# Kernel optimization log

Hardware: AMD Instinct MI355X
Metric: run time of the kernel (lower is better)

Reference implementation:

```python
import jax, jax.numpy as jnp
import numpy as np

B, S, D, H, L, V = 4, 512, 1024, 16, 4, 32000
DH = D // H
LATENT_START, N_LATENT, LATENT_ID = 64, 6, 5


def _ln(x, g, b):
    m = x.mean(-1, keepdims=True)
    v = ((x - m) ** 2).mean(-1, keepdims=True)
    return (x - m) * jax.lax.rsqrt(v + 1e-5) * g + b


def _model(x_emb, pos_ids, pos_emb, Wqkv, Wo, W1, W2, ln1_g, ln1_b, ln2_g, ln2_b, lnf_g, lnf_b, lm_head):
    # x_emb: [B,T,D]; returns (last_hidden [B,T,D] after final LN, logits [B,T,V])
    b, T, _ = x_emb.shape
    x = x_emb + pos_emb[pos_ids]
    causal = jnp.tril(jnp.ones((T, T), bool))
    for l in range(L):
        h = _ln(x, ln1_g[l], ln1_b[l])
        q, k, v = jnp.split(h @ Wqkv[l], 3, axis=-1)
        q = q.reshape(b, T, H, DH).transpose(0, 2, 1, 3)
        k = k.reshape(b, T, H, DH).transpose(0, 2, 1, 3)
        v = v.reshape(b, T, H, DH).transpose(0, 2, 1, 3)
        scores = jnp.einsum('bhqd,bhkd->bhqk', q, k) / np.float32(np.sqrt(DH))
        scores = jnp.where(causal, scores, jnp.float32(-1e9))
        attn = jax.nn.softmax(scores, axis=-1)
        o = jnp.einsum('bhqk,bhkd->bhqd', attn, v).transpose(0, 2, 1, 3).reshape(b, T, D)
        x = x + o @ Wo[l]
        h2 = _ln(x, ln2_g[l], ln2_b[l])
        x = x + jax.nn.gelu(h2 @ W1[l]) @ W2[l]
    hid = _ln(x, lnf_g, lnf_b)  # GPT2 hidden_states[-1] is post ln_f
    return hid, hid @ lm_head


def setup_inputs() -> dict:
    key = jax.random.key(0)
    ks = jax.random.split(key, 10)
    input_ids = jax.random.randint(ks[0], (B, S), 0, V, dtype=jnp.int32)
    input_ids = input_ids.at[:, LATENT_START:LATENT_START + N_LATENT].set(LATENT_ID)
    attention_mask = jnp.ones((B, S), jnp.int32)
    labels = jax.random.randint(ks[1], (B, S), 0, V, dtype=jnp.int32)
    position_ids = jnp.broadcast_to(jnp.arange(S, dtype=jnp.int32), (B, S))
    s = 0.02
    return {
        'input_ids': input_ids, 'attention_mask': attention_mask,
        'labels': labels, 'position_ids': position_ids,
        'emb': jax.random.normal(ks[2], (V, D), jnp.float32) * s,
        'pos_emb': jax.random.normal(ks[3], (S, D), jnp.float32) * s,
        'Wqkv': jax.random.normal(ks[4], (L, D, 3 * D), jnp.float32) * s,
        'Wo': jax.random.normal(ks[5], (L, D, D), jnp.float32) * s,
        'W1': jax.random.normal(ks[6], (L, D, 4 * D), jnp.float32) * s,
        'W2': jax.random.normal(ks[7], (L, 4 * D, D), jnp.float32) * s,
        'ln1_g': jnp.ones((L, D), jnp.float32), 'ln1_b': jnp.zeros((L, D), jnp.float32),
        'ln2_g': jnp.ones((L, D), jnp.float32), 'ln2_b': jnp.zeros((L, D), jnp.float32),
        'lnf_g': jnp.ones((D,), jnp.float32), 'lnf_b': jnp.zeros((D,), jnp.float32),
        'lm_head': jax.random.normal(ks[8], (D, V), jnp.float32) * s,
    }


def reference(input_ids, attention_mask, labels, position_ids, emb, pos_emb, Wqkv, Wo, W1, W2, ln1_g, ln1_b, ln2_g, ln2_b, lnf_g, lnf_b, lm_head):
    params = (pos_emb, Wqkv, Wo, W1, W2, ln1_g, ln1_b, ln2_g, ln2_b, lnf_g, lnf_b, lm_head)
    inputs_embeds = emb[input_ids]  # [B,S,D]
    start, end = 0, LATENT_START
    logits_list = []
    for p in range(N_LATENT):  # iterative latent passes
        hid, lg = _model(inputs_embeds[:, :end], position_ids[:, :end], *params)
        logits_list.append(lg[:, start:end])
        pos = LATENT_START + p
        # vectorized scatter: splice previous-position hidden state into latent slot
        inputs_embeds = inputs_embeds.at[:, pos, :].set(hid[:, pos - 1, :])
        start, end = end, (S if p + 1 >= N_LATENT else end + 1)
    hid, lg = _model(inputs_embeds[:, :end], position_ids[:, :end], *params)
    logits_list.append(lg[:, start:end])
    logits = jnp.concatenate(logits_list, axis=1)  # [B,S,V]
    shift_logits = logits[:, :-1]
    shift_labels = labels[:, 1:]
    logp = jax.nn.log_softmax(shift_logits, axis=-1)
    loss = -jnp.take_along_axis(logp, shift_labels[..., None], axis=-1).mean()
    return loss, inputs_embeds, logits
```

## Files before the change

kernel.cpp:

```cpp
#include <hip/hip_runtime.h>

static constexpr int BB  = 4;
static constexpr int SS  = 512;
static constexpr int DD  = 1024;
static constexpr int HH  = 16;
static constexpr int LL  = 4;
static constexpr int VV  = 32000;
static constexpr int DHH = 64;
static constexpr int FFF = 4096;

typedef short bf16x8  __attribute__((ext_vector_type(8)));
typedef short bf16x4v __attribute__((ext_vector_type(4)));
typedef float f32x4   __attribute__((ext_vector_type(4)));

__device__ __forceinline__ float b2f(ushort u){
  union { float f; unsigned int u32; } x; x.u32 = ((unsigned int)u) << 16; return x.f;
}
__device__ __forceinline__ ushort f2b(float f){
  union { float f; unsigned int u32; } x; x.f = f;
  unsigned int u = x.u32;
  return (ushort)((u + 0x7FFFu + ((u >> 16) & 1u)) >> 16);
}

__global__ __launch_bounds__(256) void convT_k(const float* __restrict__ in, ushort* __restrict__ out,
                                               int K, int N, long inStride, long outStride)
{
  in  += (long)blockIdx.z * inStride;
  out += (long)blockIdx.z * outStride;
  __shared__ float tile[64][65];
  int n0 = blockIdx.x * 64, k0 = blockIdx.y * 64;
  int tid = threadIdx.x;
  int cc = tid & 63, rr = tid >> 6;
#pragma unroll
  for (int i = 0; i < 16; i++){
    int r = rr + i * 4;
    tile[r][cc] = in[(long)(k0 + r) * N + n0 + cc];
  }
  __syncthreads();
#pragma unroll
  for (int i = 0; i < 16; i++){
    int r = rr + i * 4;
    out[(long)(n0 + r) * K + k0 + cc] = f2b(tile[cc][r]);
  }
}

__global__ __launch_bounds__(256) void embed_k(const int* __restrict__ ids, const float* __restrict__ emb,
                                               const float* __restrict__ pe, float* __restrict__ x,
                                               float* __restrict__ oemb)
{
  int t = blockIdx.x, b = blockIdx.y, tid = threadIdx.x;
  int id = ids[b * SS + t];
  float4 ev = *((const float4*)(emb + (long)id * DD) + tid);
  float4 pv = *((const float4*)(pe  + (long)t  * DD) + tid);
  *((float4*)(x + (long)(t * BB + b) * DD) + tid) =
      make_float4(ev.x + pv.x, ev.y + pv.y, ev.z + pv.z, ev.w + pv.w);
  float* op = oemb + ((long)b * SS + t) * DD + tid * 4;
  op[0] = ev.x; op[1] = ev.y; op[2] = ev.z; op[3] = ev.w;
}

__global__ __launch_bounds__(256) void ln_k(const float* __restrict__ xin, const float* __restrict__ g,
                                            const float* __restrict__ bt, ushort* __restrict__ out, long row0)
{
  long row = row0 + blockIdx.x;
  int tid = threadIdx.x;
  const float* rp = xin + row * DD;
  float4 v = *(const float4*)(rp + tid * 4);
  float s1 = v.x + v.y + v.z + v.w;
  float s2 = v.x * v.x + v.y * v.y + v.z * v.z + v.w * v.w;
#pragma unroll
  for (int o = 32; o; o >>= 1){ s1 += __shfl_down(s1, o); s2 += __shfl_down(s2, o); }
  __shared__ float red[2][4];
  int wv = tid >> 6, lane = tid & 63;
  if (lane == 0){ red[0][wv] = s1; red[1][wv] = s2; }
  __syncthreads();
  s1 = red[0][0] + red[0][1] + red[0][2] + red[0][3];
  s2 = red[1][0] + red[1][1] + red[1][2] + red[1][3];
  float mean = s1 * (1.0f / DD);
  float var  = s2 * (1.0f / DD) - mean * mean;
  float rstd = rsqrtf(var + 1e-5f);
  float4 gv = *(const float4*)(g + tid * 4);
  float4 bv = *(const float4*)(bt + tid * 4);
  ushort4 o4;
  o4.x = f2b((v.x - mean) * rstd * gv.x + bv.x);
  o4.y = f2b((v.y - mean) * rstd * gv.y + bv.y);
  o4.z = f2b((v.z - mean) * rstd * gv.z + bv.z);
  o4.w = f2b((v.w - mean) * rstd * gv.w + bv.w);
  *(ushort4*)(out + row * DD + tid * 4) = o4;
}

template<int EPI>
__device__ __forceinline__ void epi_store(float v, int grow, int ocol, void* Cv, int ldc,
                                          const float* Add, int t0, int l,
                                          ushort* kc, ushort* vc, ushort* qb)
{
  if constexpr (EPI == 1){
    float* Cf = (float*)Cv; long idx = (long)grow * ldc + ocol;
    Cf[idx] = v + Add[idx];
  } else if constexpr (EPI == 2){
    ushort* Cb = (ushort*)Cv; long idx = (long)grow * ldc + ocol;
    float tt = 0.7978845608028654f * (v + 0.044715f * v * v * v);
    Cb[idx] = f2b(0.5f * v * (1.0f + tanhf(tt)));
  } else if constexpr (EPI == 3){
    int t = t0 + (grow >> 2), b = grow & 3;
    ((float*)Cv)[((long)b * SS + t) * VV + ocol] = v;
  } else if constexpr (EPI == 4){
    if (ocol < DD){
      qb[((long)(t0 * BB + grow)) * DD + ocol] = f2b(v);
    } else {
      int t = t0 + (grow >> 2), b = grow & 3;
      int h = (ocol >> 6) & 15, d = ocol & 63;
      long dst = (((long)l * BB + b) * HH + h) * ((long)SS * DHH) + (long)t * DHH + d;
      if (ocol >= 2 * DD) vc[dst] = f2b(v); else kc[dst] = f2b(v);
    }
  }
}

template<int EPI>
__global__ __launch_bounds__(256) void gemm_k(const ushort* __restrict__ A, int lda,
                                              const ushort* __restrict__ BT,
                                              void* Cv, int ldc,
                                              const float* Add,
                                              int M, int N, int K, int gx,
                                              int l, int t0,
                                              ushort* kc, ushort* vc, ushort* qb,
                                              float* part, int KS)
{
  constexpr int BM  = 128;
  constexpr int MFR = 4;
  constexpr int NFR = 4;
  __shared__ ushort As[BM][72];
  __shared__ ushort Bs[128][72];
  int tid = threadIdx.x;
  int wv = tid >> 6, lane = tid & 63;
  int wm = wv >> 1, wn = wv & 1;

  int nwg = gridDim.x, orig = blockIdx.x;
  int wgid;
  if (nwg <= 1024){
    int qq = nwg >> 3, rr8 = nwg & 7, xcd = orig & 7;
    wgid = ((xcd < rr8) ? xcd * (qq + 1) : rr8 * (qq + 1) + (xcd - rr8) * qq) + (orig >> 3);
  } else {
    wgid = orig;
  }

  int gxy = gx * (N >> 7);
  int ksId = wgid / gxy;
  int rem  = wgid - ksId * gxy;
  int bx = rem % gx, by = rem / gx;
  int m0 = bx * BM, n0 = by * 128;
  int Kc = K / KS;
  int k_beg = ksId * Kc, k_end = k_beg + Kc;

  f32x4 acc[MFR][NFR];
  f32x4 zz = {0.f, 0.f, 0.f, 0.f};
#pragma unroll
  for (int m = 0; m < MFR; m++)
#pragma unroll
    for (int n = 0; n < NFR; n++) acc[m][n] = zz;

  int g4 = (lane >> 4) * 4;
  int rA = lane & 15;
  int arow = tid >> 3;
  int acol = (tid & 7) * 8;

  const ushort* Bp = BT + (long)(n0 + arow) * K + acol;
  long sB = 32 * (long)K;
  int gr0 = m0 + arow;       if (gr0 > M - 1) gr0 = M - 1;
  int gr1 = m0 + 32 + arow;  if (gr1 > M - 1) gr1 = M - 1;
  int gr2 = m0 + 64 + arow;  if (gr2 > M - 1) gr2 = M - 1;
  int gr3 = m0 + 96 + arow;  if (gr3 > M - 1) gr3 = M - 1;
  const ushort* Ap0 = A + (long)gr0 * lda + acol;
  const ushort* Ap1 = A + (long)gr1 * lda + acol;
  const ushort* Ap2 = A + (long)gr2 * lda + acol;
  const ushort* Ap3 = A + (long)gr3 * lda + acol;

  uint4 b0 = *(const uint4*)(Bp + k_beg);
  uint4 b1 = *(const uint4*)(Bp + sB + k_beg);
  uint4 b2 = *(const uint4*)(Bp + 2 * sB + k_beg);
  uint4 b3 = *(const uint4*)(Bp + 3 * sB + k_beg);
  uint4 a0 = *(const uint4*)(Ap0 + k_beg);
  uint4 a1 = *(const uint4*)(Ap1 + k_beg);
  uint4 a2 = *(const uint4*)(Ap2 + k_beg);
  uint4 a3 = *(const uint4*)(Ap3 + k_beg);

  for (int k0 = k_beg; k0 < k_end; k0 += 64){
    *(uint4*)&Bs[arow     ][acol] = b0;
    *(uint4*)&Bs[arow + 32][acol] = b1;
    *(uint4*)&Bs[arow + 64][acol] = b2;
    *(uint4*)&Bs[arow + 96][acol] = b3;
    *(uint4*)&As[arow     ][acol] = a0;
    *(uint4*)&As[arow + 32][acol] = a1;
    *(uint4*)&As[arow + 64][acol] = a2;
    *(uint4*)&As[arow + 96][acol] = a3;
    __syncthreads();
    int kn = k0 + 64;
    if (kn < k_end){
      b0 = *(const uint4*)(Bp + kn);
      b1 = *(const uint4*)(Bp + sB + kn);
      b2 = *(const uint4*)(Bp + 2 * sB + kn);
      b3 = *(const uint4*)(Bp + 3 * sB + kn);
      a0 = *(const uint4*)(Ap0 + kn);
      a1 = *(const uint4*)(Ap1 + kn);
      a2 = *(const uint4*)(Ap2 + kn);
      a3 = *(const uint4*)(Ap3 + kn);
    }
#pragma unroll
    for (int kk = 0; kk < 64; kk += 32){
      bf16x8 af[MFR], bfr[NFR];
#pragma unroll
      for (int m = 0; m < MFR; m++){
        int row = wm * 64 + m * 16 + rA;
        bf16x4v lo = *(const bf16x4v*)&As[row][kk + g4];
        bf16x4v hi = *(const bf16x4v*)&As[row][kk + 16 + g4];
        af[m] = __builtin_shufflevector(lo, hi, 0, 1, 2, 3, 4, 5, 6, 7);
      }
#pragma unroll
      for (int n = 0; n < NFR; n++){
        int row = wn * 64 + n * 16 + rA;
        bf16x4v lo = *(const bf16x4v*)&Bs[row][kk + g4];
        bf16x4v hi = *(const bf16x4v*)&Bs[row][kk + 16 + g4];
        bfr[n] = __builtin_shufflevector(lo, hi, 0, 1, 2, 3, 4, 5, 6, 7);
      }
#pragma unroll
      for (int m = 0; m < MFR; m++)
#pragma unroll
        for (int n = 0; n < NFR; n++)
          acc[m][n] = __builtin_amdgcn_mfma_f32_16x16x32_bf16(af[m], bfr[n], acc[m][n], 0, 0, 0);
    }
    __syncthreads();
  }

  int r4 = (lane >> 4) * 4;
#pragma unroll
  for (int m = 0; m < MFR; m++){
#pragma unroll
    for (int n = 0; n < NFR; n++){
      int orow = wm * 64 + m * 16 + r4;
      int ocol = n0 + wn * 64 + n * 16 + rA;
#pragma unroll
      for (int r = 0; r < 4; r++){
        int grow = m0 + orow + r;
        if (grow < M){
          if (KS > 1)
            part[(long)ksId * M * N + (long)grow * N + ocol] = acc[m][n][r];
          else
            epi_store<EPI>(acc[m][n][r], grow, ocol, Cv, ldc, Add, t0, l, kc, vc, qb);
        }
      }
    }
  }
}

__global__ __launch_bounds__(512) void gemm256_k(const ushort* __restrict__ A, int lda,
                                                 const ushort* __restrict__ BT,
                                                 float* __restrict__ Cv,
                                                 int M, int N, int K, int gx, int t0)
{
  constexpr int MFR = 4;
  constexpr int NFR = 4;
  __shared__ ushort As[128][72];
  __shared__ ushort Bs[256][72];
  int tid = threadIdx.x;
  int wv = tid >> 6, lane = tid & 63;
  int wm = wv >> 2, wn = wv & 3;

  int wgid = blockIdx.x;
  int bx = wgid % gx, by = wgid / gx;
  int m0 = bx * 128, n0 = by * 256;

  f32x4 acc[MFR][NFR];
  f32x4 zz = {0.f, 0.f, 0.f, 0.f};
#pragma unroll
  for (int m = 0; m < MFR; m++)
#pragma unroll
    for (int n = 0; n < NFR; n++) acc[m][n] = zz;

  int g4 = (lane >> 4) * 4;
  int rA = lane & 15;
  int srow = tid >> 3;
  int scol = (tid & 7) * 8;

  long sB = 64 * (long)K;
  const ushort* Bp = BT + (long)(n0 + srow) * K + scol;
  int ga0 = m0 + srow;       if (ga0 > M - 1) ga0 = M - 1;
  int ga1 = m0 + 64 + srow;  if (ga1 > M - 1) ga1 = M - 1;
  const ushort* Ap0 = A + (long)ga0 * lda + scol;
  const ushort* Ap1 = A + (long)ga1 * lda + scol;

  uint4 b0 = *(const uint4*)(Bp);
  uint4 b1 = *(const uint4*)(Bp + sB);
  uint4 b2 = *(const uint4*)(Bp + 2 * sB);
  uint4 b3 = *(const uint4*)(Bp + 3 * sB);
  uint4 a0 = *(const uint4*)(Ap0);
  uint4 a1 = *(const uint4*)(Ap1);

  for (int k0 = 0; k0 < K; k0 += 64){
    *(uint4*)&Bs[srow      ][scol] = b0;
    *(uint4*)&Bs[srow + 64 ][scol] = b1;
    *(uint4*)&Bs[srow + 128][scol] = b2;
    *(uint4*)&Bs[srow + 192][scol] = b3;
    *(uint4*)&As[srow      ][scol] = a0;
    *(uint4*)&As[srow + 64 ][scol] = a1;
    __syncthreads();
    int kn = k0 + 64;
    if (kn < K){
      b0 = *(const uint4*)(Bp + kn);
      b1 = *(const uint4*)(Bp + sB + kn);
      b2 = *(const uint4*)(Bp + 2 * sB + kn);
      b3 = *(const uint4*)(Bp + 3 * sB + kn);
      a0 = *(const uint4*)(Ap0 + kn);
      a1 = *(const uint4*)(Ap1 + kn);
    }
#pragma unroll
    for (int kk = 0; kk < 64; kk += 32){
      bf16x8 af[MFR], bfr[NFR];
#pragma unroll
      for (int m = 0; m < MFR; m++){
        int row = wm * 64 + m * 16 + rA;
        bf16x4v lo = *(const bf16x4v*)&As[row][kk + g4];
        bf16x4v hi = *(const bf16x4v*)&As[row][kk + 16 + g4];
        af[m] = __builtin_shufflevector(lo, hi, 0, 1, 2, 3, 4, 5, 6, 7);
      }
#pragma unroll
      for (int n = 0; n < NFR; n++){
        int row = wn * 64 + n * 16 + rA;
        bf16x4v lo = *(const bf16x4v*)&Bs[row][kk + g4];
        bf16x4v hi = *(const bf16x4v*)&Bs[row][kk + 16 + g4];
        bfr[n] = __builtin_shufflevector(lo, hi, 0, 1, 2, 3, 4, 5, 6, 7);
      }
#pragma unroll
      for (int m = 0; m < MFR; m++)
#pragma unroll
        for (int n = 0; n < NFR; n++)
          acc[m][n] = __builtin_amdgcn_mfma_f32_16x16x32_bf16(af[m], bfr[n], acc[m][n], 0, 0, 0);
    }
    __syncthreads();
  }

  int r4 = (lane >> 4) * 4;
#pragma unroll
  for (int m = 0; m < MFR; m++){
#pragma unroll
    for (int n = 0; n < NFR; n++){
      int orow = wm * 64 + m * 16 + r4;
      int ocol = n0 + wn * 64 + n * 16 + rA;
#pragma unroll
      for (int r = 0; r < 4; r++){
        int grow = m0 + orow + r;
        if (grow < M){
          int t = t0 + (grow >> 2), b = grow & 3;
          Cv[((long)b * SS + t) * VV + ocol] = acc[m][n][r];
        }
      }
    }
  }
}

template<int EPI>
__global__ __launch_bounds__(256) void sred_k(const float* __restrict__ part, int KS, int M, int N,
                                              void* Cv, int ldc, const float* Add,
                                              int l, int t0, ushort* kc, ushort* vc, ushort* qb)
{
  long i = (long)blockIdx.x * 256 + threadIdx.x;
  long MN = (long)M * N;
  if (i >= MN) return;
  float v = 0.f;
  for (int s = 0; s < KS; s++) v += part[s * MN + i];
  int m = (int)(i / N), n = (int)(i - (long)m * N);
  epi_store<EPI>(v, m, n, Cv, ldc, Add, t0, l, kc, vc, qb);
}

template<int TYPE>
__global__ __launch_bounds__(256) void dec_gemv_k(const float* xf, const ushort* ab,
                                                  const float* g, const float* bt,
                                                  const ushort* WT, float* x,
                                                  ushort* qb, ushort* kc, ushort* vc, ushort* gb,
                                                  int l, int pos)
{
  constexpr int K   = (TYPE == 3) ? FFF : DD;
  constexpr int NCH = K / 1024;
  int tid = threadIdx.x, wid = tid >> 6, lane = tid & 63;
  int n = blockIdx.x * 4 + wid;

  float acc[4] = {0.f, 0.f, 0.f, 0.f};

#pragma unroll
  for (int ch = 0; ch < NCH; ch++){
    int ks = ch * 1024 + lane * 16;
    float a[4][16];
    if constexpr (TYPE == 0 || TYPE == 2){
#pragma unroll
      for (int r = 0; r < 4; r++){
        const float* rp = xf + (long)(pos * BB + r) * DD + ks;
#pragma unroll
        for (int q = 0; q < 4; q++){
          float4 v = *(const float4*)(rp + q * 4);
          a[r][q*4+0] = v.x; a[r][q*4+1] = v.y; a[r][q*4+2] = v.z; a[r][q*4+3] = v.w;
        }
      }
      float gj[16], bj[16];
#pragma unroll
      for (int q = 0; q < 4; q++){
        float4 gv = *(const float4*)(g  + ks + q * 4);
        float4 bv = *(const float4*)(bt + ks + q * 4);
        gj[q*4+0]=gv.x; gj[q*4+1]=gv.y; gj[q*4+2]=gv.z; gj[q*4+3]=gv.w;
        bj[q*4+0]=bv.x; bj[q*4+1]=bv.y; bj[q*4+2]=bv.z; bj[q*4+3]=bv.w;
      }
#pragma unroll
      for (int r = 0; r < 4; r++){
        float s1 = 0.f, s2 = 0.f;
#pragma unroll
        for (int j = 0; j < 16; j++){ s1 += a[r][j]; s2 += a[r][j] * a[r][j]; }
#pragma unroll
        for (int o = 32; o; o >>= 1){ s1 += __shfl_xor(s1, o); s2 += __shfl_xor(s2, o); }
        float mean = s1 * (1.0f / DD);
        float var  = s2 * (1.0f / DD) - mean * mean;
        float rstd = rsqrtf(var + 1e-5f);
#pragma unroll
        for (int j = 0; j < 16; j++)
          a[r][j] = b2f(f2b((a[r][j] - mean) * rstd * gj[j] + bj[j]));
      }
    } else {
      constexpr int AD = (TYPE == 3) ? FFF : DD;
#pragma unroll
      for (int r = 0; r < 4; r++){
        const ushort* rp = ab + (long)(pos * BB + r) * AD + ks;
        uint4 pa = *(const uint4*)rp;
        uint4 pb = *(const uint4*)(rp + 8);
        const unsigned int w[8] = {pa.x, pa.y, pa.z, pa.w, pb.x, pb.y, pb.z, pb.w};
#pragma unroll
        for (int q = 0; q < 8; q++){
          a[r][q*2]   = b2f((ushort)(w[q] & 0xffff));
          a[r][q*2+1] = b2f((ushort)(w[q] >> 16));
        }
      }
    }
    {
      const ushort* wp = WT + (long)n * K + ks;
      uint4 pa = *(const uint4*)wp;
      uint4 pb = *(const uint4*)(wp + 8);
      const unsigned int w[8] = {pa.x, pa.y, pa.z, pa.w, pb.x, pb.y, pb.z, pb.w};
      float wf[16];
#pragma unroll
      for (int q = 0; q < 8; q++){
        wf[q*2]   = b2f((ushort)(w[q] & 0xffff));
        wf[q*2+1] = b2f((ushort)(w[q] >> 16));
      }
#pragma unroll
      for (int r = 0; r < 4; r++){
        float s = 0.f;
#pragma unroll
        for (int j = 0; j < 16; j++) s += a[r][j] * wf[j];
        acc[r] += s;
      }
    }
  }

#pragma unroll
  for (int r = 0; r < 4; r++)
#pragma unroll
    for (int o = 32; o; o >>= 1) acc[r] += __shfl_xor(acc[r], o);

  if (lane < 4){
    int r = lane;
    long Rrow = (long)(pos * BB + r);
    float v = acc[r];
    if constexpr (TYPE == 0){
      if (n < DD){
        qb[Rrow * DD + n] = f2b(v);
      } else if (n < 2 * DD){
        int h = (n - DD) >> 6, d = n & 63;
        kc[(((long)l * BB + r) * HH + h) * ((long)SS * DHH) + (long)pos * DHH + d] = f2b(v);
      } else {
        int h = (n - 2 * DD) >> 6, d = n & 63;
        vc[(((long)l * BB + r) * HH + h) * ((long)SS * DHH) + (long)pos * DHH + d] = f2b(v);
      }
    } else if constexpr (TYPE == 2){
      float tt = 0.7978845608028654f * (v + 0.044715f * v * v * v);
      gb[Rrow * FFF + n] = f2b(0.5f * v * (1.0f + tanhf(tt)));
    } else {
      long idx = Rrow * DD + n;
      x[idx] = x[idx] + v;
    }
  }
}

__global__ __launch_bounds__(256) void dec_final_k(const float* xf, const float* g, const float* bt,
                                                   const float* pe, ushort* hid, float* x,
                                                   float* oemb, int pos)
{
  int wid = threadIdx.x >> 6, lane = threadIdx.x & 63;
  long R = (long)(pos * BB + wid);
  const float* rp = xf + R * DD + lane * 16;
  float a[16];
#pragma unroll
  for (int q = 0; q < 4; q++){
    float4 v = *(const float4*)(rp + q * 4);
    a[q*4+0] = v.x; a[q*4+1] = v.y; a[q*4+2] = v.z; a[q*4+3] = v.w;
  }
  float s1 = 0.f, s2 = 0.f;
#pragma unroll
  for (int j = 0; j < 16; j++){ s1 += a[j]; s2 += a[j] * a[j]; }
#pragma unroll
  for (int o = 32; o; o >>= 1){ s1 += __shfl_xor(s1, o); s2 += __shfl_xor(s2, o); }
  float mean = s1 * (1.0f / DD);
  float var  = s2 * (1.0f / DD) - mean * mean;
  float rstd = rsqrtf(var + 1e-5f);
  int pn = pos + 1;
#pragma unroll
  for (int j = 0; j < 16; j++){
    int d = lane * 16 + j;
    ushort hb = f2b((a[j] - mean) * rstd * g[d] + bt[d]);
    hid[R * DD + d] = hb;
    float hv = b2f(hb);
    oemb[((long)wid * SS + pn) * DD + d] = hv;
    x[((long)(pn * BB + wid)) * DD + d] = hv + pe[(long)pn * DD + d];
  }
}

__global__ __launch_bounds__(256) void attn_k(const ushort* __restrict__ qb, const ushort* __restrict__ kc,
                                              const ushort* __restrict__ vc, ushort* __restrict__ o,
                                              int l, int t0, int Tc)
{
  __shared__ float sc[4][512];
  __shared__ float qs[4][64];
  int tid = threadIdx.x, wv = tid >> 6, lane = tid & 63;
  int b = blockIdx.z, h = blockIdx.y;
  int qrow = blockIdx.x * 4 + wv;
  bool act = qrow < Tc;
  int tq = t0 + qrow;
  long kvoff = (((long)l * BB + b) * HH + h) * ((long)SS * DHH);
  const ushort* kb = kc + kvoff;
  const ushort* vb = vc + kvoff;
  if (act) qs[wv][lane] = b2f(qb[((long)(tq * BB + b)) * DD + h * DHH + lane]);
  __syncthreads();
  int nk = act ? (tq + 1) : 0;
  float m = -3.0e38f;
  for (int key = lane; key < nk; key += 64){
    const ushort* kp = kb + (long)key * DHH;
    float s = 0.f;
#pragma unroll
    for (int j = 0; j < 8; j++){
      uint4 kvv = *(const uint4*)(kp + j * 8);
      s += qs[wv][j*8+0] * b2f((ushort)(kvv.x & 0xffff));
      s += qs[wv][j*8+1] * b2f((ushort)(kvv.x >> 16));
      s += qs[wv][j*8+2] * b2f((ushort)(kvv.y & 0xffff));
      s += qs[wv][j*8+3] * b2f((ushort)(kvv.y >> 16));
      s += qs[wv][j*8+4] * b2f((ushort)(kvv.z & 0xffff));
      s += qs[wv][j*8+5] * b2f((ushort)(kvv.z >> 16));
      s += qs[wv][j*8+6] * b2f((ushort)(kvv.w & 0xffff));
      s += qs[wv][j*8+7] * b2f((ushort)(kvv.w >> 16));
    }
    s *= 0.125f;
    sc[wv][key] = s;
    m = fmaxf(m, s);
  }
#pragma unroll
  for (int off = 32; off; off >>= 1) m = fmaxf(m, __shfl_xor(m, off));
  float ssum = 0.f;
  for (int key = lane; key < nk; key += 64){
    float p = expf(sc[wv][key] - m);
    sc[wv][key] = p;
    ssum += p;
  }
#pragma unroll
  for (int off = 32; off; off >>= 1) ssum += __shfl_xor(ssum, off);
  __syncthreads();
  float accv = 0.f;
  int key = 0;
  for (; key + 3 < nk; key += 4){
    float p0 = sc[wv][key],     p1 = sc[wv][key + 1];
    float p2 = sc[wv][key + 2], p3 = sc[wv][key + 3];
    float v0 = b2f(vb[(long)key * DHH + lane]);
    float v1 = b2f(vb[(long)(key + 1) * DHH + lane]);
    float v2 = b2f(vb[(long)(key + 2) * DHH + lane]);
    float v3 = b2f(vb[(long)(key + 3) * DHH + lane]);
    accv += p0 * v0 + p1 * v1 + p2 * v2 + p3 * v3;
  }
  for (; key < nk; key++)
    accv += sc[wv][key] * b2f(vb[(long)key * DHH + lane]);
  if (act) o[((long)(tq * BB + b)) * DD + h * DHH + lane] = f2b(accv / ssum);
}

__global__ __launch_bounds__(256) void advance_k(const ushort* __restrict__ hid, const float* __restrict__ pe,
                                                 float* __restrict__ x, float* __restrict__ oemb, int pos)
{
  int d = blockIdx.x * 256 + threadIdx.x;
  int b = blockIdx.y;
  float hv = b2f(hid[((long)((pos - 1) * BB + b)) * DD + d]);
  oemb[((long)b * SS + pos) * DD + d] = hv;
  x[((long)(pos * BB + b)) * DD + d] = hv + pe[(long)pos * DD + d];
}

__global__ __launch_bounds__(256) void loss_rows_k(const float* __restrict__ logits, const int* __restrict__ labels,
                                                   float* __restrict__ rowloss)
{
  int t = blockIdx.x, b = blockIdx.y, tid = threadIdx.x;
  const float* row = logits + ((long)b * SS + t) * VV;
  float m = -3.0e38f, s = 0.f;
  auto upd = [&](float v){
    if (v > m){ s = s * expf(m - v) + 1.f; m = v; }
    else s += expf(v - m);
  };
  if (tid < 3) upd(row[tid]);
  if (tid == 3) upd(row[VV - 1]);
  const float4* vrow = (const float4*)(row + 3);
  for (int i = tid; i < 7999; i += 256){
    float4 v = vrow[i];
    upd(v.x); upd(v.y); upd(v.z); upd(v.w);
  }
#pragma unroll
  for (int off = 32; off; off >>= 1){
    float om = __shfl_xor(m, off), os = __shfl_xor(s, off);
    float nm = fmaxf(m, om);
    s = s * expf(m - nm) + os * expf(om - nm);
    m = nm;
  }
  __shared__ float sm[4], ssb[4];
  if ((tid & 63) == 0){ sm[tid >> 6] = m; ssb[tid >> 6] = s; }
  __syncthreads();
  if (tid == 0){
    float M = fmaxf(fmaxf(sm[0], sm[1]), fmaxf(sm[2], sm[3]));
    float S = ssb[0] * expf(sm[0] - M) + ssb[1] * expf(sm[1] - M)
            + ssb[2] * expf(sm[2] - M) + ssb[3] * expf(sm[3] - M);
    int lab = labels[b * SS + t + 1];
    rowloss[b * (SS - 1) + t] = (M + logf(S)) - row[lab];
  }
}

__global__ __launch_bounds__(256) void loss_final_k(const float* __restrict__ rowloss, float* __restrict__ out)
{
  int tid = threadIdx.x;
  float s = 0.f;
  for (int i = tid; i < BB * (SS - 1); i += 256) s += rowloss[i];
#pragma unroll
  for (int o = 32; o; o >>= 1) s += __shfl_down(s, o);
  __shared__ float red[4];
  if ((tid & 63) == 0) red[tid >> 6] = s;
  __syncthreads();
  if (tid == 0) out[0] = (red[0] + red[1] + red[2] + red[3]) / (float)(BB * (SS - 1));
}

static inline int cdiv_i(int a, int b){ return (a + b - 1) / b; }

extern "C" void kernel_launch(void* const* d_in, const int* in_sizes, int n_in,
                              void* d_out, int out_size, void* d_ws, size_t ws_size,
                              hipStream_t stream)
{
  (void)in_sizes; (void)n_in; (void)out_size; (void)ws_size;
  const int*   ids    = (const int*)d_in[0];
  const int*   labels = (const int*)d_in[2];
  const float* emb    = (const float*)d_in[4];
  const float* pe     = (const float*)d_in[5];
  const float* Wqkv   = (const float*)d_in[6];
  const float* Wo     = (const float*)d_in[7];
  const float* W1     = (const float*)d_in[8];
  const float* W2     = (const float*)d_in[9];
  const float* ln1g   = (const float*)d_in[10];
  const float* ln1b   = (const float*)d_in[11];
  const float* ln2g   = (const float*)d_in[12];
  const float* ln2b   = (const float*)d_in[13];
  const float* lnfg   = (const float*)d_in[14];
  const float* lnfb   = (const float*)d_in[15];
  const float* lm     = (const float*)d_in[16];

  float* out_loss   = (float*)d_out;
  float* out_emb    = out_loss + 1;
  float* out_logits = out_emb + (size_t)BB * SS * DD;

  char* wsp = (char*)d_ws;
  size_t off = 0;
  auto alloc = [&](size_t bytes) -> void* {
    void* p = wsp + off; off += (bytes + 255) & ~(size_t)255; return p;
  };
  ushort* wqkvT = (ushort*)alloc((size_t)LL * 3 * DD * DD * 2);
  ushort* woT   = (ushort*)alloc((size_t)LL * DD * DD * 2);
  ushort* w1T   = (ushort*)alloc((size_t)LL * FFF * DD * 2);
  ushort* w2T   = (ushort*)alloc((size_t)LL * DD * FFF * 2);
  ushort* lmT   = (ushort*)alloc((size_t)VV * DD * 2);
  float*  x     = (float*)alloc((size_t)BB * SS * DD * 4);
  ushort* hbuf  = (ushort*)alloc((size_t)BB * SS * DD * 2);
  ushort* qbuf  = (ushort*)alloc((size_t)BB * SS * DD * 2);
  ushort* obuf  = (ushort*)alloc((size_t)BB * SS * DD * 2);
  ushort* gbuf  = (ushort*)alloc((size_t)BB * SS * FFF * 2);
  ushort* hid   = (ushort*)alloc((size_t)BB * SS * DD * 2);
  ushort* kcache= (ushort*)alloc((size_t)LL * BB * SS * DD * 2);
  ushort* vcache= (ushort*)alloc((size_t)LL * BB * SS * DD * 2);
  float*  rowls = (float*)alloc((size_t)BB * (SS - 1) * 4);
  float*  part  = out_logits;

  convT_k<<<dim3(3 * DD / 64, DD / 64, LL), dim3(256), 0, stream>>>(Wqkv, wqkvT, DD, 3 * DD, (long)DD * 3 * DD, (long)3 * DD * DD);
  convT_k<<<dim3(DD / 64, DD / 64, LL),     dim3(256), 0, stream>>>(Wo,   woT,  DD, DD,     (long)DD * DD,     (long)DD * DD);
  convT_k<<<dim3(FFF / 64, DD / 64, LL),    dim3(256), 0, stream>>>(W1,   w1T,  DD, FFF,    (long)DD * FFF,    (long)FFF * DD);
  convT_k<<<dim3(DD / 64, FFF / 64, LL),    dim3(256), 0, stream>>>(W2,   w2T,  FFF, DD,    (long)FFF * DD,    (long)DD * FFF);
  convT_k<<<dim3(VV / 64, DD / 64, 1),      dim3(256), 0, stream>>>(lm,   lmT,  DD, VV,     0, 0);

  embed_k<<<dim3(SS, BB), dim3(256), 0, stream>>>(ids, emb, pe, x, out_emb);

  const int ct0[7] = {0, 64, 65, 66, 67, 68, 69};
  const int ct1[7] = {64, 65, 66, 67, 68, 69, 512};

  auto g128 = [&](int epi, const ushort* A, int lda, const ushort* BT, void* C, int ldc,
                  const float* Add, int M, int N, int K, int l, int t0, int KS){
    int gx = cdiv_i(M, 128);
    int nwg = gx * (N >> 7) * KS;
    if (epi == 1) gemm_k<1><<<nwg, 256, 0, stream>>>(A, lda, BT, C, ldc, Add, M, N, K, gx, l, t0, kcache, vcache, qbuf, part, KS);
    if (epi == 2) gemm_k<2><<<nwg, 256, 0, stream>>>(A, lda, BT, C, ldc, Add, M, N, K, gx, l, t0, kcache, vcache, qbuf, part, KS);
    if (epi == 3) gemm_k<3><<<nwg, 256, 0, stream>>>(A, lda, BT, C, ldc, Add, M, N, K, gx, l, t0, kcache, vcache, qbuf, part, KS);
    if (epi == 4) gemm_k<4><<<nwg, 256, 0, stream>>>(A, lda, BT, C, ldc, Add, M, N, K, gx, l, t0, kcache, vcache, qbuf, part, KS);
    if (KS > 1){
      int nred = cdiv_i(M * N, 256);
      if (epi == 1) sred_k<1><<<nred, 256, 0, stream>>>(part, KS, M, N, C, ldc, Add, l, t0, kcache, vcache, qbuf);
      if (epi == 2) sred_k<2><<<nred, 256, 0, stream>>>(part, KS, M, N, C, ldc, Add, l, t0, kcache, vcache, qbuf);
      if (epi == 4) sred_k<4><<<nred, 256, 0, stream>>>(part, KS, M, N, C, ldc, Add, l, t0, kcache, vcache, qbuf);
    }
  };

  for (int c = 0; c < 7; c++){
    int t0 = ct0[c];
    int Tc = ct1[c] - t0;
    int M  = Tc * BB;
    long roff = (long)t0 * BB;

    if (Tc == 1){
      int pos = t0;
      for (int l = 0; l < LL; l++){
        dec_gemv_k<0><<<dim3(3 * DD / 4), dim3(256), 0, stream>>>(x, nullptr, ln1g + l * DD, ln1b + l * DD,
            wqkvT + (long)l * 3 * DD * DD, nullptr, qbuf, kcache, vcache, nullptr, l, pos);
        attn_k<<<dim3(1, HH, BB), dim3(64), 0, stream>>>(qbuf, kcache, vcache, obuf, l, t0, Tc);
        dec_gemv_k<1><<<dim3(DD / 4), dim3(256), 0, stream>>>(nullptr, obuf, nullptr, nullptr,
            woT + (long)l * DD * DD, x, nullptr, nullptr, nullptr, nullptr, l, pos);
        dec_gemv_k<2><<<dim3(FFF / 4), dim3(256), 0, stream>>>(x, nullptr, ln2g + l * DD, ln2b + l * DD,
            w1T + (long)l * FFF * DD, nullptr, nullptr, nullptr, nullptr, gbuf, l, pos);
        dec_gemv_k<3><<<dim3(DD / 4), dim3(256), 0, stream>>>(nullptr, gbuf, nullptr, nullptr,
            w2T + (long)l * DD * FFF, x, nullptr, nullptr, nullptr, nullptr, l, pos);
      }
      dec_final_k<<<dim3(1), dim3(256), 0, stream>>>(x, lnfg, lnfb, pe, hid, x, out_emb, pos);
    } else {
      bool small = (M <= 256);
      int ksQKV = small ? 4 : 1;
      int ksWO  = small ? 8 : 2;
      int ksW1  = small ? 4 : 1;
      int ksW2  = small ? 8 : 2;
      for (int l = 0; l < LL; l++){
        ln_k<<<dim3(M), dim3(256), 0, stream>>>(x, ln1g + l * DD, ln1b + l * DD, hbuf, roff);
        g128(4, hbuf + roff * DD, DD, wqkvT + (long)l * 3 * DD * DD, nullptr, 0, nullptr, M, 3 * DD, DD, l, t0, ksQKV);
        attn_k<<<dim3(cdiv_i(Tc, 4), HH, BB), dim3(256), 0, stream>>>(qbuf, kcache, vcache, obuf, l, t0, Tc);
        g128(1, obuf + roff * DD, DD, woT + (long)l * DD * DD, x + roff * DD, DD, x + roff * DD, M, DD, DD, l, t0, ksWO);
        ln_k<<<dim3(M), dim3(256), 0, stream>>>(x, ln2g + l * DD, ln2b + l * DD, hbuf, roff);
        g128(2, hbuf + roff * DD, DD, w1T + (long)l * FFF * DD, gbuf + roff * FFF, FFF, nullptr, M, FFF, DD, l, t0, ksW1);
        g128(1, gbuf + roff * FFF, FFF, w2T + (long)l * DD * FFF, x + roff * DD, DD, x + roff * DD, M, DD, FFF, l, t0, ksW2);
      }
      ln_k<<<dim3(M), dim3(256), 0, stream>>>(x, lnfg, lnfb, hid, roff);
      if (c == 0)
        advance_k<<<dim3(DD / 256, BB), dim3(256), 0, stream>>>(hid, pe, x, out_emb, 64);
    }
  }

  {
    int gx = BB * SS / 128;
    int nwg = gx * (VV / 256);
    gemm256_k<<<nwg, 512, 0, stream>>>(hid, DD, lmT, out_logits, BB * SS, VV, DD, gx, 0);
  }

  loss_rows_k<<<dim3(SS - 1, BB), dim3(256), 0, stream>>>(out_logits, labels, rowls);
  loss_final_k<<<dim3(1), dim3(256), 0, stream>>>(rowls, out_loss);
}
```

Baseline: 2.879 ms.

## Rewrite LM-head GEMM with direct global-to-LDS double buffering and XOR-swizzled LDS

The final vocabulary projection GEMM now loads tiles straight from global memory into LDS using the global_load_lds builtin, double-buffers those tiles so the next K-tile loads while the current one is computed, and XOR-swizzles the LDS layout to avoid bank conflicts without padding. The tile shrinks from 128x256 with 512 threads to 128x128 with 256 threads, which doubles the workgroup count. The split-K partial buffer moves from the logits output into its own workspace allocation. This targets global-load latency and register-staging overhead in the largest GEMM, at the cost of less B-tile reuse per block.

```diff
diff --git a/kernel.cpp b/kernel.cpp
--- a/kernel.cpp
+++ b/kernel.cpp
@@ -20,6 +20,16 @@
   union { float f; unsigned int u32; } x; x.f = f;
   unsigned int u = x.u32;
   return (ushort)((u + 0x7FFFu + ((u >> 16) & 1u)) >> 16);
+}
+
+__device__ __forceinline__ void gl_lds16(const void* gp, void* lp){
+  __builtin_amdgcn_global_load_lds((const __attribute__((address_space(1))) unsigned int*)gp,
+                                   (__attribute__((address_space(3))) unsigned int*)lp, 16, 0, 0);
+}
+
+__device__ __forceinline__ bf16x4v lds_read4(const void* buf, int row, int col){
+  int byte = row * 128 + (((((col >> 3) ^ (row & 7)) << 4) | ((col & 7) << 1)));
+  return *(const bf16x4v*)((const char*)buf + byte);
 }
 
 __global__ __launch_bounds__(256) void convT_k(const float* __restrict__ in, ushort* __restrict__ out,
@@ -251,22 +261,22 @@
   }
 }
 
-__global__ __launch_bounds__(512) void gemm256_k(const ushort* __restrict__ A, int lda,
-                                                 const ushort* __restrict__ BT,
-                                                 float* __restrict__ Cv,
-                                                 int M, int N, int K, int gx, int t0)
+__global__ __launch_bounds__(256) void gemm2p_k(const ushort* __restrict__ A, int lda,
+                                                const ushort* __restrict__ BT,
+                                                float* __restrict__ Cf,
+                                                int M, int N, int K, int gx, int t0)
 {
   constexpr int MFR = 4;
   constexpr int NFR = 4;
-  __shared__ ushort As[128][72];
-  __shared__ ushort Bs[256][72];
+  __shared__ ushort As[2][128][64];
+  __shared__ ushort Bs[2][128][64];
   int tid = threadIdx.x;
   int wv = tid >> 6, lane = tid & 63;
-  int wm = wv >> 2, wn = wv & 3;
+  int wm = wv >> 1, wn = wv & 1;
 
   int wgid = blockIdx.x;
   int bx = wgid % gx, by = wgid / gx;
-  int m0 = bx * 128, n0 = by * 256;
+  int m0 = bx * 128, n0 = by * 128;
 
   f32x4 acc[MFR][NFR];
   f32x4 zz = {0.f, 0.f, 0.f, 0.f};
@@ -277,55 +287,56 @@
 
   int g4 = (lane >> 4) * 4;
   int rA = lane & 15;
-  int srow = tid >> 3;
-  int scol = (tid & 7) * 8;
-
-  long sB = 64 * (long)K;
-  const ushort* Bp = BT + (long)(n0 + srow) * K + scol;
-  int ga0 = m0 + srow;       if (ga0 > M - 1) ga0 = M - 1;
-  int ga1 = m0 + 64 + srow;  if (ga1 > M - 1) ga1 = M - 1;
-  const ushort* Ap0 = A + (long)ga0 * lda + scol;
-  const ushort* Ap1 = A + (long)ga1 * lda + scol;
-
-  uint4 b0 = *(const uint4*)(Bp);
-  uint4 b1 = *(const uint4*)(Bp + sB);
-  uint4 b2 = *(const uint4*)(Bp + 2 * sB);
-  uint4 b3 = *(const uint4*)(Bp + 3 * sB);
-  uint4 a0 = *(const uint4*)(Ap0);
-  uint4 a1 = *(const uint4*)(Ap1);
-
-  for (int k0 = 0; k0 < K; k0 += 64){
-    *(uint4*)&Bs[srow      ][scol] = b0;
-    *(uint4*)&Bs[srow + 64 ][scol] = b1;
-    *(uint4*)&Bs[srow + 128][scol] = b2;
-    *(uint4*)&Bs[srow + 192][scol] = b3;
-    *(uint4*)&As[srow      ][scol] = a0;
-    *(uint4*)&As[srow + 64 ][scol] = a1;
-    __syncthreads();
-    int kn = k0 + 64;
-    if (kn < K){
-      b0 = *(const uint4*)(Bp + kn);
-      b1 = *(const uint4*)(Bp + sB + kn);
-      b2 = *(const uint4*)(Bp + 2 * sB + kn);
-      b3 = *(const uint4*)(Bp + 3 * sB + kn);
-      a0 = *(const uint4*)(Ap0 + kn);
-      a1 = *(const uint4*)(Ap1 + kn);
-    }
+  int arow = tid >> 3;
+  int acol = (((tid & 7) ^ (arow & 7)) * 8);
+
+  const ushort* Bp = BT + (long)(n0 + arow) * K + acol;
+  long sB = 32 * (long)K;
+  int gr0 = m0 + arow;       if (gr0 > M - 1) gr0 = M - 1;
+  int gr1 = m0 + 32 + arow;  if (gr1 > M - 1) gr1 = M - 1;
+  int gr2 = m0 + 64 + arow;  if (gr2 > M - 1) gr2 = M - 1;
+  int gr3 = m0 + 96 + arow;  if (gr3 > M - 1) gr3 = M - 1;
+  const ushort* Ap0 = A + (long)gr0 * lda + acol;
+  const ushort* Ap1 = A + (long)gr1 * lda + acol;
+  const ushort* Ap2 = A + (long)gr2 * lda + acol;
+  const ushort* Ap3 = A + (long)gr3 * lda + acol;
+
+  auto stage = [&](int buf, int k0){
+    char* AsB = (char*)&As[buf][0][0];
+    char* BsB = (char*)&Bs[buf][0][0];
+    gl_lds16(Bp + k0,          BsB + tid * 16);
+    gl_lds16(Bp + sB + k0,     BsB + 4096 + tid * 16);
+    gl_lds16(Bp + 2 * sB + k0, BsB + 8192 + tid * 16);
+    gl_lds16(Bp + 3 * sB + k0, BsB + 12288 + tid * 16);
+    gl_lds16(Ap0 + k0,         AsB + tid * 16);
+    gl_lds16(Ap1 + k0,         AsB + 4096 + tid * 16);
+    gl_lds16(Ap2 + k0,         AsB + 8192 + tid * 16);
+    gl_lds16(Ap3 + k0,         AsB + 12288 + tid * 16);
+  };
+
+  int NT = K >> 6;
+  stage(0, 0);
+  __syncthreads();
+  int cur = 0;
+  for (int t = 0; t < NT; t++){
+    if (t + 1 < NT) stage(cur ^ 1, (t + 1) << 6);
+    const char* AsB = (const char*)&As[cur][0][0];
+    const char* BsB = (const char*)&Bs[cur][0][0];
 #pragma unroll
     for (int kk = 0; kk < 64; kk += 32){
       bf16x8 af[MFR], bfr[NFR];
 #pragma unroll
       for (int m = 0; m < MFR; m++){
         int row = wm * 64 + m * 16 + rA;
-        bf16x4v lo = *(const bf16x4v*)&As[row][kk + g4];
-        bf16x4v hi = *(const bf16x4v*)&As[row][kk + 16 + g4];
+        bf16x4v lo = lds_read4(AsB, row, kk + g4);
+        bf16x4v hi = lds_read4(AsB, row, kk + 16 + g4);
         af[m] = __builtin_shufflevector(lo, hi, 0, 1, 2, 3, 4, 5, 6, 7);
       }
 #pragma unroll
       for (int n = 0; n < NFR; n++){
         int row = wn * 64 + n * 16 + rA;
-        bf16x4v lo = *(const bf16x4v*)&Bs[row][kk + g4];
-        bf16x4v hi = *(const bf16x4v*)&Bs[row][kk + 16 + g4];
+        bf16x4v lo = lds_read4(BsB, row, kk + g4);
+        bf16x4v hi = lds_read4(BsB, row, kk + 16 + g4);
         bfr[n] = __builtin_shufflevector(lo, hi, 0, 1, 2, 3, 4, 5, 6, 7);
       }
 #pragma unroll
@@ -335,6 +346,7 @@
           acc[m][n] = __builtin_amdgcn_mfma_f32_16x16x32_bf16(af[m], bfr[n], acc[m][n], 0, 0, 0);
     }
     __syncthreads();
+    cur ^= 1;
   }
 
   int r4 = (lane >> 4) * 4;
@@ -349,7 +361,7 @@
         int grow = m0 + orow + r;
         if (grow < M){
           int t = t0 + (grow >> 2), b = grow & 3;
-          Cv[((long)b * SS + t) * VV + ocol] = acc[m][n][r];
+          Cf[((long)b * SS + t) * VV + ocol] = acc[m][n][r];
         }
       }
     }
@@ -686,8 +698,8 @@
   ushort* hid   = (ushort*)alloc((size_t)BB * SS * DD * 2);
   ushort* kcache= (ushort*)alloc((size_t)LL * BB * SS * DD * 2);
   ushort* vcache= (ushort*)alloc((size_t)LL * BB * SS * DD * 2);
+  float*  part  = (float*)alloc((size_t)17 * 1024 * 1024);
   float*  rowls = (float*)alloc((size_t)BB * (SS - 1) * 4);
-  float*  part  = out_logits;
 
   convT_k<<<dim3(3 * DD / 64, DD / 64, LL), dim3(256), 0, stream>>>(Wqkv, wqkvT, DD, 3 * DD, (long)DD * 3 * DD, (long)3 * DD * DD);
   convT_k<<<dim3(DD / 64, DD / 64, LL),     dim3(256), 0, stream>>>(Wo,   woT,  DD, DD,     (long)DD * DD,     (long)DD * DD);
@@ -759,8 +771,8 @@
 
   {
     int gx = BB * SS / 128;
-    int nwg = gx * (VV / 256);
-    gemm256_k<<<nwg, 512, 0, stream>>>(hid, DD, lmT, out_logits, BB * SS, VV, DD, gx, 0);
+    int nwg = gx * (VV >> 7);
+    gemm2p_k<<<nwg, 256, 0, stream>>>(hid, DD, lmT, out_logits, BB * SS, VV, DD, gx, 0);
   }
 
   loss_rows_k<<<dim3(SS - 1, BB), dim3(256), 0, stream>>>(out_logits, labels, rowls);
```

Measured after the change: 2.865 ms. Within noise of the previous version (-0.5%).
